# Optimization experiments

Hardware: AMD Instinct MI355X
Metric: run time of the kernel (lower is better)

The kernel has to match this reference:

```python
import jax, jax.numpy as jnp
import numpy as np

N_USERS = 100000
N_ITEMS = 50000
N_NODES = N_USERS + N_ITEMS
NNZ = 4800000
EMB_DIM = 64
N_LAYERS = 3
MASK_PROB = 0.2


def setup_inputs() -> dict:
    key = jax.random.key(0)
    k1, k2, k3, k4, k5, k6, k7 = jax.random.split(key, 7)
    user_emb = jax.random.normal(k1, (N_USERS, EMB_DIM), dtype=jnp.float32) * 0.1
    item_emb = jax.random.normal(k2, (N_ITEMS, EMB_DIM), dtype=jnp.float32) * 0.1
    adj_rows = jax.random.randint(k3, (NNZ,), 0, N_NODES, dtype=jnp.int32)
    adj_cols = jax.random.randint(k4, (NNZ,), 0, N_NODES, dtype=jnp.int32)
    # positive normalization weights (stand-in for D^-1/2 A D^-1/2 values)
    adj_vals = jax.random.uniform(k5, (NNZ,), dtype=jnp.float32) * (1.0 / 32.0)
    # deterministic Bernoulli(1 - MASK_PROB) mask, same math as tf.random.uniform > mask_prob
    mask = (jax.random.uniform(k6, (N_USERS, EMB_DIM)) > MASK_PROB).astype(jnp.float32)
    kw, kb = jax.random.split(k7)
    limit = np.sqrt(6.0 / (EMB_DIM + EMB_DIM)).astype(np.float32)  # Glorot uniform
    attr_W = jax.random.uniform(kw, (EMB_DIM, EMB_DIM), minval=-limit, maxval=limit, dtype=jnp.float32)
    attr_b = jnp.zeros((EMB_DIM,), dtype=jnp.float32)
    return {"user_emb": user_emb, "item_emb": item_emb, "adj_rows": adj_rows,
            "adj_cols": adj_cols, "adj_vals": adj_vals, "mask": mask,
            "attr_W": attr_W, "attr_b": attr_b}


def _spmm(rows, cols, vals, x):
    # y[r] = sum_{e: rows[e]==r} vals[e] * x[cols[e]]
    gathered = x[cols] * vals[:, None]            # [nnz, d]
    return jax.ops.segment_sum(gathered, rows, num_segments=N_NODES)


def reference(user_emb, item_emb, adj_rows, adj_cols, adj_vals, mask, attr_W, attr_b):
    all_emb = jnp.concatenate([user_emb, item_emb], axis=0)  # [N, d]
    acc = all_emb
    h = all_emb
    for _ in range(N_LAYERS):
        h = _spmm(adj_rows, adj_cols, adj_vals, h)
        acc = acc + h
    combined = acc * (1.0 / (N_LAYERS + 1))                  # uniform alpha_k
    user_final = combined[:N_USERS]
    item_final = combined[N_USERS:]
    masked_user_emb = user_final * mask
    predicted_attributes = jax.nn.relu(masked_user_emb @ attr_W + attr_b)
    return (user_final, item_final, masked_user_emb, predicted_attributes, mask)
```

## Files before the change

### kernel.cpp

```cpp
#include <hip/hip_runtime.h>

constexpr int NU = 100000;
constexpr int NI = 50000;
constexpr int NN = 150000;
constexpr int EMB = 64;
constexpr size_t U64 = (size_t)NU * EMB;
constexpr size_t N64 = (size_t)NN * EMB;
constexpr int BKR = 1024;
constexpr int NBC = (NN + BKR - 1) / BKR;
constexpr int CHUNK_A = 4864;
constexpr int CHUNK_H = 32768;

__device__ inline unsigned int bfp(float a, float b) {
    unsigned int ua = __float_as_uint(a), ub = __float_as_uint(b);
    ua += 0x7fffu + ((ua >> 16) & 1u);
    ub += 0x7fffu + ((ub >> 16) & 1u);
    return (ua >> 16) | (ub & 0xffff0000u);
}
__device__ inline float blo(unsigned int u) { return __uint_as_float(u << 16); }
__device__ inline float bhi(unsigned int u) { return __uint_as_float(u & 0xffff0000u); }


__global__ void zero_k(int* __restrict__ p, int n) {
    int i = blockIdx.x * blockDim.x + threadIdx.x;
    if (i < n) p[i] = 0;
}

__global__ __launch_bounds__(1024) void chist_k(const int* __restrict__ rows,
                                                int* __restrict__ bcnt, int nnz) {
    __shared__ int lh[NBC];
    int t = threadIdx.x;
    if (t < NBC) lh[t] = 0;
    __syncthreads();
    int cb = blockIdx.x * CHUNK_H;
    int ce = min(cb + CHUNK_H, nnz);
    for (int i = cb + t; i < ce; i += 1024) atomicAdd(&lh[rows[i] >> 10], 1);
    __syncthreads();
    if (t < NBC) {
        int v = lh[t];
        if (v) atomicAdd(&bcnt[t], v);
    }
}

__global__ __launch_bounds__(256) void bscan_k(const int* __restrict__ bcnt,
                                               int* __restrict__ bbase,
                                               int* __restrict__ gcur, int nnz) {
    __shared__ int part[256];
    int t = threadIdx.x;
    int v = (t < NBC) ? bcnt[t] : 0;
    part[t] = v;
    __syncthreads();
    for (int d = 1; d < 256; d <<= 1) {
        int u = (t >= d) ? part[t - d] : 0;
        __syncthreads();
        part[t] += u;
        __syncthreads();
    }
    if (t < NBC) {
        int e = part[t] - v;
        bbase[t] = e;
        gcur[t] = e;
    }
    if (t == 0) bbase[NBC] = nnz;
}

__global__ __launch_bounds__(1024) void passA_k(const int* __restrict__ rows,
                                                const int* __restrict__ cols,
                                                const float* __restrict__ vals,
                                                int* __restrict__ gcur,
                                                int2* __restrict__ stage, int nnz) {
    __shared__ int lhist[NBC];
    __shared__ int shiftb[NBC];
    __shared__ int lcur[NBC];
    __shared__ int part[1024];
    __shared__ int2 ebuf[CHUNK_A];
    __shared__ int eshift[CHUNK_A];
    int t = threadIdx.x;
    int cb = blockIdx.x * CHUNK_A;
    int ce = min(cb + CHUNK_A, nnz);
    if (t < NBC) lhist[t] = 0;
    __syncthreads();
    for (int i = cb + t; i < ce; i += 1024) atomicAdd(&lhist[rows[i] >> 10], 1);
    __syncthreads();
    part[t] = (t < NBC) ? lhist[t] : 0;
    __syncthreads();
    for (int d = 1; d < 1024; d <<= 1) {
        int v = (t >= d) ? part[t - d] : 0;
        __syncthreads();
        part[t] += v;
        __syncthreads();
    }
    if (t < NBC) {
        int cnt = lhist[t];
        int lo = part[t] - cnt;
        lcur[t] = lo;
        int gb = cnt ? atomicAdd(&gcur[t], cnt) : 0;
        shiftb[t] = gb - lo;
    }
    __syncthreads();
    for (int i = cb + t; i < ce; i += 1024) {
        int r = rows[i];
        int bk = r >> 10;
        int d = atomicAdd(&lcur[bk], 1);
        ebuf[d] = make_int2(cols[i] | ((r & 1023) << 18), __float_as_int(vals[i]));
        eshift[d] = shiftb[bk];
    }
    __syncthreads();
    int n = ce - cb;
    for (int dst = t; dst < n; dst += 1024) {
        stage[eshift[dst] + dst] = ebuf[dst];
    }
}

__global__ __launch_bounds__(1024) void passB_k(const int2* __restrict__ stage,
                                                const int* __restrict__ bbase,
                                                int* __restrict__ offs,
                                                int2* __restrict__ edges) {
    __shared__ int part[1024];
    __shared__ int lcur[1024];
    int b = blockIdx.x;
    int t = threadIdx.x;
    int beg = bbase[b];
    int end = bbase[b + 1];
    lcur[t] = 0;
    __syncthreads();
    for (int i = beg + t; i < end; i += 1024) {
        atomicAdd(&lcur[(stage[i].x >> 18) & 1023], 1);
    }
    __syncthreads();
    int v = lcur[t];
    part[t] = v;
    __syncthreads();
    for (int d = 1; d < 1024; d <<= 1) {
        int u = (t >= d) ? part[t - d] : 0;
        __syncthreads();
        part[t] += u;
        __syncthreads();
    }
    int rowoff = beg + part[t] - v;
    lcur[t] = rowoff;
    offs[b * 1024 + t] = rowoff;
    __syncthreads();
    for (int i = beg + t; i < end; i += 1024) {
        int2 e = stage[i];
        int lrow = (e.x >> 18) & 1023;
        int pos = atomicAdd(&lcur[lrow], 1);
        edges[pos] = make_int2(e.x & 0x3ffff, e.y);
    }
}

__global__ void init_k(const float4* __restrict__ ue, const float4* __restrict__ ie,
                       float4* __restrict__ acc, uint2* __restrict__ hb0) {
    int i = blockIdx.x * blockDim.x + threadIdx.x;
    const int n4 = (int)(N64 / 4);
    if (i >= n4) return;
    const int u4 = (int)(U64 / 4);
    float4 v = (i < u4) ? ue[i] : ie[i - u4];
    acc[i] = v;
    hb0[i] = make_uint2(bfp(v.x, v.y), bfp(v.z, v.w));
}

template<int MODE>
__global__ __launch_bounds__(256) void spmm_g(
    const int* __restrict__ offs, const int2* __restrict__ edges,
    const unsigned int* __restrict__ xb, uint2* __restrict__ yb, float4* __restrict__ acc,
    const float4* __restrict__ mask, float4* __restrict__ masked,
    float4* __restrict__ mout) {
    int w = (blockIdx.x * 256 + (int)threadIdx.x) >> 6;
    int lane = threadIdx.x & 63;
    if (w >= NN) return;
    int beg = offs[w], end = offs[w + 1];
    int g = lane >> 4, gl = lane & 15;
    float4 s = make_float4(0.f, 0.f, 0.f, 0.f);
    for (int p = beg; p < end; p += 32) {
        int idx = p + lane;
        int2 e = (lane < 32 && idx < end) ? edges[idx] : make_int2(0, 0);
        #pragma unroll
        for (int j = 0; j < 8; ++j) {
            int src = g * 8 + j;
            int c = __shfl(e.x, src);
            float v = __int_as_float(__shfl(e.y, src));
            uint2 u = *(const uint2*)(xb + (size_t)c * 32 + gl * 2);
            s.x += v * blo(u.x); s.y += v * bhi(u.x);
            s.z += v * blo(u.y); s.w += v * bhi(u.y);
        }
    }
    #pragma unroll
    for (int d = 16; d <= 32; d <<= 1) {
        s.x += __shfl_xor(s.x, d);
        s.y += __shfl_xor(s.y, d);
        s.z += __shfl_xor(s.z, d);
        s.w += __shfl_xor(s.w, d);
    }
    if (lane < 16) {
        size_t o = (size_t)w * 16 + gl;
        if (MODE == 0) {
            yb[o] = make_uint2(bfp(s.x, s.y), bfp(s.z, s.w));
            float4 a = acc[o];
            acc[o] = make_float4(a.x + s.x, a.y + s.y, a.z + s.z, a.w + s.w);
        } else if (MODE == 1) {
            yb[o] = make_uint2(bfp(s.x, s.y), bfp(s.z, s.w));
        } else {
            uint2 h2 = *(const uint2*)(xb + (size_t)w * 32 + gl * 2);
            float4 a = acc[o];
            float4 c = make_float4((a.x + blo(h2.x) + s.x) * 0.25f,
                                   (a.y + bhi(h2.x) + s.y) * 0.25f,
                                   (a.z + blo(h2.y) + s.z) * 0.25f,
                                   (a.w + bhi(h2.y) + s.w) * 0.25f);
            acc[o] = c;
            if (w < NU) {
                float4 m = mask[o];
                masked[o] = make_float4(c.x * m.x, c.y * m.y, c.z * m.z, c.w * m.w);
                mout[o] = m;
            }
        }
    }
}

__global__ __launch_bounds__(256) void attr_gemm_k(const float* __restrict__ masked,
                                                   const float* __restrict__ W,
                                                   const float* __restrict__ bias,
                                                   float* __restrict__ out) {
    __shared__ float mt[64][68];
    __shared__ float Wt[64][68];
    __shared__ float bl[64];
    int t = threadIdx.x;
    int rowbase = blockIdx.x * 64;
    const float4* W4 = (const float4*)W;
    #pragma unroll
    for (int j = 0; j < 4; ++j) {
        int idx = t + 256 * j;
        float4 w = W4[idx];
        *(float4*)&Wt[idx >> 4][(idx & 15) * 4] = w;
    }
    if (t < 64) bl[t] = bias[t];
    const float4* M4 = (const float4*)(masked + (size_t)rowbase * 64);
    #pragma unroll
    for (int j = 0; j < 4; ++j) {
        int idx = t + 256 * j;
        float4 m = M4[idx];
        *(float4*)&mt[idx >> 4][(idx & 15) * 4] = m;
    }
    __syncthreads();
    int r0 = (t >> 4) * 4, c0 = (t & 15) * 4;
    float a0x = 0, a0y = 0, a0z = 0, a0w = 0;
    float a1x = 0, a1y = 0, a1z = 0, a1w = 0;
    float a2x = 0, a2y = 0, a2z = 0, a2w = 0;
    float a3x = 0, a3y = 0, a3z = 0, a3w = 0;
    #pragma unroll 8
    for (int k = 0; k < 64; ++k) {
        float4 wv = *(const float4*)&Wt[k][c0];
        float m0 = mt[r0 + 0][k];
        float m1 = mt[r0 + 1][k];
        float m2 = mt[r0 + 2][k];
        float m3 = mt[r0 + 3][k];
        a0x += m0 * wv.x; a0y += m0 * wv.y; a0z += m0 * wv.z; a0w += m0 * wv.w;
        a1x += m1 * wv.x; a1y += m1 * wv.y; a1z += m1 * wv.z; a1w += m1 * wv.w;
        a2x += m2 * wv.x; a2y += m2 * wv.y; a2z += m2 * wv.z; a2w += m2 * wv.w;
        a3x += m3 * wv.x; a3y += m3 * wv.y; a3z += m3 * wv.z; a3w += m3 * wv.w;
    }
    float4 bv = *(const float4*)&bl[c0];
    float rx[4][4] = {{a0x, a0y, a0z, a0w}, {a1x, a1y, a1z, a1w},
                      {a2x, a2y, a2z, a2w}, {a3x, a3y, a3z, a3w}};
    #pragma unroll
    for (int i = 0; i < 4; ++i) {
        int r = rowbase + r0 + i;
        if (r < NU) {
            float4 o;
            o.x = fmaxf(rx[i][0] + bv.x, 0.f);
            o.y = fmaxf(rx[i][1] + bv.y, 0.f);
            o.z = fmaxf(rx[i][2] + bv.z, 0.f);
            o.w = fmaxf(rx[i][3] + bv.w, 0.f);
            *(float4*)&out[(size_t)r * 64 + c0] = o;
        }
    }
}


__global__ void finit_k(const float4* __restrict__ ue, const float4* __restrict__ ie,
                        float4* __restrict__ acc, float4* __restrict__ h0,
                        float4* __restrict__ h1) {
    int i = blockIdx.x * blockDim.x + threadIdx.x;
    const int n4 = (int)(N64 / 4);
    if (i >= n4) return;
    const int u4 = (int)(U64 / 4);
    float4 v = (i < u4) ? ue[i] : ie[i - u4];
    acc[i] = v; h0[i] = v; h1[i] = make_float4(0.f, 0.f, 0.f, 0.f);
}

__global__ void spmm_atomic_k(const int* __restrict__ rows, const int* __restrict__ cols,
                              const float* __restrict__ vals,
                              const float* __restrict__ x, float* __restrict__ y, int nnz) {
    int e = (blockIdx.x * blockDim.x + threadIdx.x) >> 6;
    int lane = threadIdx.x & 63;
    if (e >= nnz) return;
    int r = rows[e]; int c = cols[e]; float v = vals[e];
    atomicAdd(&y[(size_t)r * EMB + lane], x[(size_t)c * EMB + lane] * v);
}

__global__ void addzero_k(float4* __restrict__ acc, const float4* __restrict__ hin,
                          float4* __restrict__ hz) {
    int i = blockIdx.x * blockDim.x + threadIdx.x;
    const int n4 = (int)(N64 / 4);
    if (i >= n4) return;
    float4 a = acc[i]; float4 b = hin[i];
    a.x += b.x; a.y += b.y; a.z += b.z; a.w += b.w;
    acc[i] = a; hz[i] = make_float4(0.f, 0.f, 0.f, 0.f);
}

__global__ void final_k(float4* __restrict__ acc_io, const float4* __restrict__ hlast,
                        const float4* __restrict__ mask, float4* __restrict__ masked_out) {
    int i = blockIdx.x * blockDim.x + threadIdx.x;
    const int n4 = (int)(N64 / 4);
    if (i >= n4) return;
    float4 a = acc_io[i]; float4 h = hlast[i];
    float4 c = make_float4((a.x + h.x) * 0.25f, (a.y + h.y) * 0.25f,
                           (a.z + h.z) * 0.25f, (a.w + h.w) * 0.25f);
    acc_io[i] = c;
    const int u4 = (int)(U64 / 4);
    if (i < u4) {
        float4 m = mask[i];
        masked_out[i] = make_float4(c.x * m.x, c.y * m.y, c.z * m.z, c.w * m.w);
    }
}

__global__ void copy_k(const float4* __restrict__ src, float4* __restrict__ dst, int n4) {
    int i = blockIdx.x * blockDim.x + threadIdx.x;
    if (i < n4) dst[i] = src[i];
}


extern "C" void kernel_launch(void* const* d_in, const int* in_sizes, int n_in,
                              void* d_out, int out_size, void* d_ws, size_t ws_size,
                              hipStream_t stream) {
    const float* user_emb = (const float*)d_in[0];
    const float* item_emb = (const float*)d_in[1];
    const int*   rows     = (const int*)d_in[2];
    const int*   cols     = (const int*)d_in[3];
    const float* vals     = (const float*)d_in[4];
    const float* mask     = (const float*)d_in[5];
    const float* W        = (const float*)d_in[6];
    const float* b        = (const float*)d_in[7];
    float* out = (float*)d_out;
    const int nnz = in_sizes[2];

    float* acc = out;
    float* masked_out = out + N64;
    float* pred_out   = out + N64 + U64;
    float* mask_out   = out + N64 + 2 * U64;

    const int blk = 256;
    const int n4 = (int)(N64 / 4);
    const int grid_n4 = (n4 + blk - 1) / blk;
    const int u4 = (int)(U64 / 4);
    const int grid_attr = (NU + 63) / 64;

    int* bcnt  = (int*)d_ws;
    int* bbase = bcnt + 256;
    int* gcur  = bbase + 256;
    int* offs  = gcur + 256;
    int2* edges = (int2*)(offs + 150784);
    const size_t need = (256 * 3 + 150784) * 4 + (size_t)nnz * 8 + 64;

    if (ws_size >= need) {
        int2* stage = (int2*)(out + N64);
        uint2* hb0 = (uint2*)(out + N64 + U64);
        uint2* hb1 = hb0 + (N64 / 4);

        zero_k<<<1, 256, 0, stream>>>(bcnt, 256);
        chist_k<<<(nnz + CHUNK_H - 1) / CHUNK_H, 1024, 0, stream>>>(rows, bcnt, nnz);
        bscan_k<<<1, 256, 0, stream>>>(bcnt, bbase, gcur, nnz);
        passA_k<<<(nnz + CHUNK_A - 1) / CHUNK_A, 1024, 0, stream>>>(rows, cols, vals,
                                                                    gcur, stage, nnz);
        passB_k<<<NBC, 1024, 0, stream>>>(stage, bbase, offs, edges);

        init_k<<<grid_n4, blk, 0, stream>>>((const float4*)user_emb,
                                            (const float4*)item_emb,
                                            (float4*)acc, hb0);

        const int grid_sp = (int)(((size_t)NN * 64) / blk);
        spmm_g<0><<<grid_sp, blk, 0, stream>>>(offs, edges, (const unsigned int*)hb0,
                                               hb1, (float4*)acc,
                                               nullptr, nullptr, nullptr);
        spmm_g<1><<<grid_sp, blk, 0, stream>>>(offs, edges, (const unsigned int*)hb1,
                                               hb0, (float4*)acc,
                                               nullptr, nullptr, nullptr);
        spmm_g<2><<<grid_sp, blk, 0, stream>>>(offs, edges, (const unsigned int*)hb0,
                                               nullptr, (float4*)acc,
                                               (const float4*)mask, (float4*)masked_out,
                                               (float4*)mask_out);

        attr_gemm_k<<<grid_attr, blk, 0, stream>>>(masked_out, W, b, pred_out);
    } else {
        float* h0 = out + N64;
        float* h1 = out + 2 * N64;
        finit_k<<<grid_n4, blk, 0, stream>>>((const float4*)user_emb,
                                             (const float4*)item_emb,
                                             (float4*)acc, (float4*)h0, (float4*)h1);
        const long long st = (long long)nnz * 64;
        const int grid_sc = (int)((st + blk - 1) / blk);
        spmm_atomic_k<<<grid_sc, blk, 0, stream>>>(rows, cols, vals, h0, h1, nnz);
        addzero_k<<<grid_n4, blk, 0, stream>>>((float4*)acc, (const float4*)h1, (float4*)h0);
        spmm_atomic_k<<<grid_sc, blk, 0, stream>>>(rows, cols, vals, h1, h0, nnz);
        addzero_k<<<grid_n4, blk, 0, stream>>>((float4*)acc, (const float4*)h0, (float4*)h1);
        spmm_atomic_k<<<grid_sc, blk, 0, stream>>>(rows, cols, vals, h0, h1, nnz);
        final_k<<<grid_n4, blk, 0, stream>>>((float4*)acc, (const float4*)h1,
                                             (const float4*)mask, (float4*)masked_out);
        attr_gemm_k<<<grid_attr, blk, 0, stream>>>(masked_out, W, b, pred_out);
        copy_k<<<(u4 + blk - 1) / blk, blk, 0, stream>>>((const float4*)mask,
                                                         (float4*)mask_out, u4);
    }
}
```

Measured before the change: 431.6 us.

## Quantize propagated embeddings to per-row int8 instead of bf16 in SpMM

Replaces the bf16 storage of intermediate layer embeddings with per-row symmetric int8 quantization (offset-128 bytes plus one float scale per row). The SpMM gather then reads 64 bytes per neighbor row instead of 128, plus a scale load, which halves the main random-gather traffic. The cost is extra dequantize/quantize arithmetic, a wave-level max reduction on every output row, and much coarser precision, so the output may drift from the reference tolerance.

```diff
diff --git a/kernel.cpp b/kernel.cpp
--- a/kernel.cpp
+++ b/kernel.cpp
@@ -11,14 +11,13 @@
 constexpr int CHUNK_A = 4864;
 constexpr int CHUNK_H = 32768;
 
-__device__ inline unsigned int bfp(float a, float b) {
-    unsigned int ua = __float_as_uint(a), ub = __float_as_uint(b);
-    ua += 0x7fffu + ((ua >> 16) & 1u);
-    ub += 0x7fffu + ((ub >> 16) & 1u);
-    return (ua >> 16) | (ub & 0xffff0000u);
-}
-__device__ inline float blo(unsigned int u) { return __uint_as_float(u << 16); }
-__device__ inline float bhi(unsigned int u) { return __uint_as_float(u & 0xffff0000u); }
+__device__ inline unsigned int pack8(float x, float y, float z, float w, float inv) {
+    int b0 = (int)rintf(fminf(fmaxf(x * inv, -127.f), 127.f)) + 128;
+    int b1 = (int)rintf(fminf(fmaxf(y * inv, -127.f), 127.f)) + 128;
+    int b2 = (int)rintf(fminf(fmaxf(z * inv, -127.f), 127.f)) + 128;
+    int b3 = (int)rintf(fminf(fmaxf(w * inv, -127.f), 127.f)) + 128;
+    return (unsigned)b0 | ((unsigned)b1 << 8) | ((unsigned)b2 << 16) | ((unsigned)b3 << 24);
+}
 
 
 __global__ void zero_k(int* __restrict__ p, int n) {
@@ -149,21 +148,31 @@
     }
 }
 
-__global__ void init_k(const float4* __restrict__ ue, const float4* __restrict__ ie,
-                       float4* __restrict__ acc, uint2* __restrict__ hb0) {
-    int i = blockIdx.x * blockDim.x + threadIdx.x;
-    const int n4 = (int)(N64 / 4);
-    if (i >= n4) return;
-    const int u4 = (int)(U64 / 4);
-    float4 v = (i < u4) ? ue[i] : ie[i - u4];
-    acc[i] = v;
-    hb0[i] = make_uint2(bfp(v.x, v.y), bfp(v.z, v.w));
+__global__ __launch_bounds__(256) void init8_k(const float4* __restrict__ ue,
+                                               const float4* __restrict__ ie,
+                                               float4* __restrict__ acc,
+                                               unsigned int* __restrict__ hb,
+                                               float* __restrict__ hsc) {
+    int row = blockIdx.x * 16 + (threadIdx.x >> 4);
+    int gl = threadIdx.x & 15;
+    if (row >= NN) return;
+    const float4* src = (row < NU) ? (ue + (size_t)row * 16)
+                                   : (ie + (size_t)(row - NU) * 16);
+    float4 v = src[gl];
+    acc[(size_t)row * 16 + gl] = v;
+    float am = fmaxf(fmaxf(fabsf(v.x), fabsf(v.y)), fmaxf(fabsf(v.z), fabsf(v.w)));
+    #pragma unroll
+    for (int d = 1; d <= 8; d <<= 1) am = fmaxf(am, __shfl_xor(am, d));
+    float inv = (am > 0.f) ? 127.f / am : 0.f;
+    hb[(size_t)row * 16 + gl] = pack8(v.x, v.y, v.z, v.w, inv);
+    if (gl == 0) hsc[row] = am * (1.f / 127.f);
 }
 
 template<int MODE>
 __global__ __launch_bounds__(256) void spmm_g(
     const int* __restrict__ offs, const int2* __restrict__ edges,
-    const unsigned int* __restrict__ xb, uint2* __restrict__ yb, float4* __restrict__ acc,
+    const unsigned int* __restrict__ xb, const float* __restrict__ xsc,
+    unsigned int* __restrict__ yb, float* __restrict__ ysc, float4* __restrict__ acc,
     const float4* __restrict__ mask, float4* __restrict__ masked,
     float4* __restrict__ mout) {
     int w = (blockIdx.x * 256 + (int)threadIdx.x) >> 6;
@@ -172,6 +181,7 @@
     int beg = offs[w], end = offs[w + 1];
     int g = lane >> 4, gl = lane & 15;
     float4 s = make_float4(0.f, 0.f, 0.f, 0.f);
+    float C = 0.f;
     for (int p = beg; p < end; p += 32) {
         int idx = p + lane;
         int2 e = (lane < 32 && idx < end) ? edges[idx] : make_int2(0, 0);
@@ -180,11 +190,17 @@
             int src = g * 8 + j;
             int c = __shfl(e.x, src);
             float v = __int_as_float(__shfl(e.y, src));
-            uint2 u = *(const uint2*)(xb + (size_t)c * 32 + gl * 2);
-            s.x += v * blo(u.x); s.y += v * bhi(u.x);
-            s.z += v * blo(u.y); s.w += v * bhi(u.y);
+            unsigned int u = xb[(size_t)c * 16 + gl];
+            float sc = xsc[c] * v;
+            C += sc;
+            s.x += sc * (float)(u & 0xffu);
+            s.y += sc * (float)((u >> 8) & 0xffu);
+            s.z += sc * (float)((u >> 16) & 0xffu);
+            s.w += sc * (float)(u >> 24);
         }
     }
+    float bias = 128.f * C;
+    s.x -= bias; s.y -= bias; s.z -= bias; s.w -= bias;
     #pragma unroll
     for (int d = 16; d <= 32; d <<= 1) {
         s.x += __shfl_xor(s.x, d);
@@ -194,19 +210,30 @@
     }
     if (lane < 16) {
         size_t o = (size_t)w * 16 + gl;
-        if (MODE == 0) {
-            yb[o] = make_uint2(bfp(s.x, s.y), bfp(s.z, s.w));
+        if (MODE == 0 || MODE == 1) {
+            float am = fmaxf(fmaxf(fabsf(s.x), fabsf(s.y)),
+                             fmaxf(fabsf(s.z), fabsf(s.w)));
+            #pragma unroll
+            for (int d = 1; d <= 8; d <<= 1) am = fmaxf(am, __shfl_xor(am, d));
+            float inv = (am > 0.f) ? 127.f / am : 0.f;
+            yb[o] = pack8(s.x, s.y, s.z, s.w, inv);
+            if (gl == 0) ysc[w] = am * (1.f / 127.f);
+            if (MODE == 0) {
+                float4 a = acc[o];
+                acc[o] = make_float4(a.x + s.x, a.y + s.y, a.z + s.z, a.w + s.w);
+            }
+        } else {
+            unsigned int u2 = xb[(size_t)w * 16 + gl];
+            float sc2 = xsc[w];
+            float h0 = ((float)(u2 & 0xffu) - 128.f) * sc2;
+            float h1 = ((float)((u2 >> 8) & 0xffu) - 128.f) * sc2;
+            float h2 = ((float)((u2 >> 16) & 0xffu) - 128.f) * sc2;
+            float h3 = ((float)(u2 >> 24) - 128.f) * sc2;
             float4 a = acc[o];
-            acc[o] = make_float4(a.x + s.x, a.y + s.y, a.z + s.z, a.w + s.w);
-        } else if (MODE == 1) {
-            yb[o] = make_uint2(bfp(s.x, s.y), bfp(s.z, s.w));
-        } else {
-            uint2 h2 = *(const uint2*)(xb + (size_t)w * 32 + gl * 2);
-            float4 a = acc[o];
-            float4 c = make_float4((a.x + blo(h2.x) + s.x) * 0.25f,
-                                   (a.y + bhi(h2.x) + s.y) * 0.25f,
-                                   (a.z + blo(h2.y) + s.z) * 0.25f,
-                                   (a.w + bhi(h2.y) + s.w) * 0.25f);
+            float4 c = make_float4((a.x + h0 + s.x) * 0.25f,
+                                   (a.y + h1 + s.y) * 0.25f,
+                                   (a.z + h2 + s.z) * 0.25f,
+                                   (a.w + h3 + s.w) * 0.25f);
             acc[o] = c;
             if (w < NU) {
                 float4 m = mask[o];
@@ -364,8 +391,10 @@
 
     if (ws_size >= need) {
         int2* stage = (int2*)(out + N64);
-        uint2* hb0 = (uint2*)(out + N64 + U64);
-        uint2* hb1 = hb0 + (N64 / 4);
+        unsigned int* hb8_0 = (unsigned int*)(out + N64 + U64);
+        unsigned int* hb8_1 = hb8_0 + (N64 / 4);
+        float* sc0 = (float*)(hb8_1 + (N64 / 4));
+        float* sc1 = sc0 + 150016;
 
         zero_k<<<1, 256, 0, stream>>>(bcnt, 256);
         chist_k<<<(nnz + CHUNK_H - 1) / CHUNK_H, 1024, 0, stream>>>(rows, bcnt, nnz);
@@ -374,19 +403,19 @@
                                                                     gcur, stage, nnz);
         passB_k<<<NBC, 1024, 0, stream>>>(stage, bbase, offs, edges);
 
-        init_k<<<grid_n4, blk, 0, stream>>>((const float4*)user_emb,
-                                            (const float4*)item_emb,
-                                            (float4*)acc, hb0);
+        init8_k<<<(NN + 15) / 16, blk, 0, stream>>>((const float4*)user_emb,
+                                                    (const float4*)item_emb,
+                                                    (float4*)acc, hb8_0, sc0);
 
         const int grid_sp = (int)(((size_t)NN * 64) / blk);
-        spmm_g<0><<<grid_sp, blk, 0, stream>>>(offs, edges, (const unsigned int*)hb0,
-                                               hb1, (float4*)acc,
+        spmm_g<0><<<grid_sp, blk, 0, stream>>>(offs, edges, hb8_0, sc0,
+                                               hb8_1, sc1, (float4*)acc,
                                                nullptr, nullptr, nullptr);
-        spmm_g<1><<<grid_sp, blk, 0, stream>>>(offs, edges, (const unsigned int*)hb1,
-                                               hb0, (float4*)acc,
+        spmm_g<1><<<grid_sp, blk, 0, stream>>>(offs, edges, hb8_1, sc1,
+                                               hb8_0, sc0, (float4*)acc,
                                                nullptr, nullptr, nullptr);
-        spmm_g<2><<<grid_sp, blk, 0, stream>>>(offs, edges, (const unsigned int*)hb0,
-                                               nullptr, (float4*)acc,
+        spmm_g<2><<<grid_sp, blk, 0, stream>>>(offs, edges, hb8_0, sc0,
+                                               nullptr, nullptr, (float4*)acc,
                                                (const float4*)mask, (float4*)masked_out,
                                                (float4*)mask_out);
 
```

New measurement: 411.0 us. -4.8%, faster.
